# Optimization experiments

Measured on AMD Instinct MI355X. Metric: run time of the kernel, lower is better.

## Reference

```python
import jax, jax.numpy as jnp
import numpy as np

B_COEF = 1.0  # b in __init__
F_POW = 1     # f in __init__
H_POW = 2     # h in __init__
N_NODES = 16384
DIM = 16


def setup_inputs() -> dict:
    key = jax.random.key(0)
    kA, kx = jax.random.split(key)
    # Adjacency with nonnegative entries (dense, as in the torch dense branch)
    A = jax.random.uniform(kA, (N_NODES, N_NODES), dtype=jnp.float32)
    x = jax.random.uniform(kx, (N_NODES, DIM), dtype=jnp.float32)
    return {"A": A, "x": x, "t": 0}


def reference(A, x, t):
    # dx/dt = -b * x^f + (A @ x^h) / (x^h + 1)
    # NOTE: python precedence in the original: (A @ x**h) / (x**h + 1)
    xh = x ** H_POW            # [n, dim]
    agg = A @ xh               # [n, dim] adjacency aggregation
    return -B_COEF * x ** F_POW + agg / (xh + 1.0)
```

## Files before the change

kernel.cpp:

```cpp
#include <hip/hip_runtime.h>
#include <stdint.h>


#define NN 16384
#define DIM 16
#define TPB 256
#define ROWS 32
#define NRB 512
#define KSPLIT 2
#define KRANGE 8192
#define KC 256
#define NCH 32

__global__ __launch_bounds__(256) void prep_kernel(const float* __restrict__ x,
                                                   float* __restrict__ out,
                                                   float* __restrict__ xh,
                                                   float* __restrict__ inv) {
    int i = blockIdx.x * 256 + threadIdx.x;
    float4 v = reinterpret_cast<const float4*>(x)[i];
    reinterpret_cast<float4*>(out)[i] = make_float4(-v.x, -v.y, -v.z, -v.w);
    float4 h = make_float4(v.x * v.x, v.y * v.y, v.z * v.z, v.w * v.w);
    reinterpret_cast<float4*>(xh)[i] = h;
    reinterpret_cast<float4*>(inv)[i] =
        make_float4(1.0f / (h.x + 1.0f), 1.0f / (h.y + 1.0f),
                    1.0f / (h.z + 1.0f), 1.0f / (h.w + 1.0f));
}

__device__ __forceinline__ void gload_lds16(const float* g, float* l, int aux) {
    if (aux)
        __builtin_amdgcn_global_load_lds(
            (const __attribute__((address_space(1))) void*)g,
            (__attribute__((address_space(3))) void*)l, 16, 0, 2 );
    else
        __builtin_amdgcn_global_load_lds(
            (const __attribute__((address_space(1))) void*)g,
            (__attribute__((address_space(3))) void*)l, 16, 0, 0);
}

__global__ __launch_bounds__(TPB) void agg_kernel(const float* __restrict__ A,
                                                  const float* __restrict__ xh,
                                                  const float* __restrict__ inv,
                                                  float* __restrict__ out) {
    __shared__ float tA[ROWS * KC];
    __shared__ float tX[KC * DIM];

    const int tid = threadIdx.x;
    const int l = tid & 63, w = tid >> 6, m = l & 15, q = l >> 4;
    const int rb = blockIdx.x & (NRB - 1);
    const int ks = blockIdx.x >> 9;
    const int r0 = rb * ROWS;
    const size_t k0 = (size_t)ks * KRANGE;

    const float* Ab = A + (size_t)(r0 + 8 * w) * NN + k0;
    int aoff[8];
    #pragma unroll
    for (int i = 0; i < 8; ++i) aoff[i] = 4 * (l ^ (i & 7));

    const float* Xc = xh + k0 * DIM;
    int xoff[4];
    #pragma unroll
    for (int j = 0; j < 4; ++j)
        xoff[j] = (((4 * w + j) * 16 + (l >> 2)) << 4) + 4 * ((l & 3) ^ j);

    int rA[2][4];
    #pragma unroll
    for (int j = 0; j < 2; ++j)
        #pragma unroll
        for (int b = 0; b < 4; ++b)
            rA[j][b] = (m + 16 * j) * KC + 4 * ((16 * w + 4 * q + b) ^ (m & 7));
    int rX[4];
    #pragma unroll
    for (int v = 0; v < 4; ++v)
        rX[v] = (64 * w + 16 * q) * 16 + 4 * (v ^ ((4 * w + q) & 3));

    float4 acc[2][4];
    #pragma unroll
    for (int j = 0; j < 2; ++j)
        #pragma unroll
        for (int v = 0; v < 4; ++v) acc[j][v] = make_float4(0.f, 0.f, 0.f, 0.f);

    for (int t = 0; t < NCH; ++t) {
        __syncthreads();
        {
            const float* sA = Ab + (size_t)t * KC;
            #pragma unroll
            for (int i = 0; i < 8; ++i)
                gload_lds16(sA + (size_t)i * NN + aoff[i],
                            &tA[(8 * w + i) * KC], 1);
            const float* sX = Xc + (size_t)t * (KC * DIM);
            #pragma unroll
            for (int j = 0; j < 4; ++j)
                gload_lds16(sX + xoff[j], &tX[(4 * w + j) * 256], 0);
        }
        __syncthreads();
        #pragma unroll
        for (int b = 0; b < 4; ++b) {
            float4 ar[2];
            ar[0] = *reinterpret_cast<const float4*>(&tA[rA[0][b]]);
            ar[1] = *reinterpret_cast<const float4*>(&tA[rA[1][b]]);
            #pragma unroll
            for (int e = 0; e < 4; ++e) {
                float4 xv[4];
                #pragma unroll
                for (int v = 0; v < 4; ++v)
                    xv[v] = *reinterpret_cast<const float4*>(
                        &tX[rX[v] + (4 * b + e) * 16]);
                #pragma unroll
                for (int j = 0; j < 2; ++j) {
                    const float a = (&ar[j].x)[e];
                    #pragma unroll
                    for (int v = 0; v < 4; ++v) {
                        acc[j][v].x += a * xv[v].x;
                        acc[j][v].y += a * xv[v].y;
                        acc[j][v].z += a * xv[v].z;
                        acc[j][v].w += a * xv[v].w;
                    }
                }
            }
        }
    }

    #pragma unroll
    for (int j = 0; j < 2; ++j)
        #pragma unroll
        for (int v = 0; v < 4; ++v) {
            acc[j][v].x += __shfl_xor(acc[j][v].x, 16);
            acc[j][v].y += __shfl_xor(acc[j][v].y, 16);
            acc[j][v].z += __shfl_xor(acc[j][v].z, 16);
            acc[j][v].w += __shfl_xor(acc[j][v].w, 16);
            acc[j][v].x += __shfl_xor(acc[j][v].x, 32);
            acc[j][v].y += __shfl_xor(acc[j][v].y, 32);
            acc[j][v].z += __shfl_xor(acc[j][v].z, 32);
            acc[j][v].w += __shfl_xor(acc[j][v].w, 32);
        }

    if (q == 0) {
        #pragma unroll
        for (int j = 0; j < 2; ++j) {
            const int R = r0 + m + 16 * j;
            const float4* iv4 = reinterpret_cast<const float4*>(inv + (size_t)R * DIM);
            float* orow = out + (size_t)R * DIM;
            #pragma unroll
            for (int v = 0; v < 4; ++v) {
                float4 iv = iv4[v];
                atomicAdd(&orow[4 * v + 0], acc[j][v].x * iv.x);
                atomicAdd(&orow[4 * v + 1], acc[j][v].y * iv.y);
                atomicAdd(&orow[4 * v + 2], acc[j][v].z * iv.z);
                atomicAdd(&orow[4 * v + 3], acc[j][v].w * iv.w);
            }
        }
    }
}

extern "C" void kernel_launch(void* const* d_in, const int* in_sizes, int n_in,
                              void* d_out, int out_size, void* d_ws, size_t ws_size,
                              hipStream_t stream) {
    const float* A = (const float*)d_in[0];
    const float* x = (const float*)d_in[1];
    float* out = (float*)d_out;
    float* xhp = (float*)d_ws;
    float* inv = (float*)d_ws + (size_t)NN * DIM;

    prep_kernel<<<(NN * DIM / 4) / 256, 256, 0, stream>>>(x, out, xhp, inv);
    agg_kernel<<<NRB * KSPLIT, TPB, 0, stream>>>(A, xhp, inv, out);
}
```

Measured before the change: 296.1 us.

## Remap thread tile to 4 rows x 8 k-slices and use butterfly reduction

```diff
diff --git a/kernel.cpp b/kernel.cpp
--- a/kernel.cpp
+++ b/kernel.cpp
@@ -26,8 +26,8 @@
                     1.0f / (h.z + 1.0f), 1.0f / (h.w + 1.0f));
 }
 
-__device__ __forceinline__ void gload_lds16(const float* g, float* l, int aux) {
-    if (aux)
+__device__ __forceinline__ void gload_lds16(const void* g, void* l, int nt) {
+    if (nt)
         __builtin_amdgcn_global_load_lds(
             (const __attribute__((address_space(1))) void*)g,
             (__attribute__((address_space(3))) void*)l, 16, 0, 2 );
@@ -37,15 +37,23 @@
             (__attribute__((address_space(3))) void*)l, 16, 0, 0);
 }
 
-__global__ __launch_bounds__(TPB) void agg_kernel(const float* __restrict__ A,
-                                                  const float* __restrict__ xh,
-                                                  const float* __restrict__ inv,
-                                                  float* __restrict__ out) {
+__device__ __forceinline__ float4 shfl_xor4(float4 v, int mask) {
+    return make_float4(__shfl_xor(v.x, mask), __shfl_xor(v.y, mask),
+                       __shfl_xor(v.z, mask), __shfl_xor(v.w, mask));
+}
+
+__global__ __launch_bounds__(TPB)
+__attribute__((amdgpu_waves_per_eu(1, 3)))
+void agg_kernel(const float* __restrict__ A,
+                const float* __restrict__ xh,
+                const float* __restrict__ inv,
+                float* __restrict__ out) {
     __shared__ float tA[ROWS * KC];
     __shared__ float tX[KC * DIM];
 
     const int tid = threadIdx.x;
-    const int l = tid & 63, w = tid >> 6, m = l & 15, q = l >> 4;
+    const int l = tid & 63, w = tid >> 6;
+    const int m8 = l & 7, q8 = l >> 3;
     const int rb = blockIdx.x & (NRB - 1);
     const int ks = blockIdx.x >> 9;
     const int r0 = rb * ROWS;
@@ -59,23 +67,19 @@
     const float* Xc = xh + k0 * DIM;
     int xoff[4];
     #pragma unroll
+    for (int j = 0; j < 4; ++j) xoff[j] = (4 * w + j) * 256 + 4 * l;
+
+    int rA[4][2];
+    #pragma unroll
     for (int j = 0; j < 4; ++j)
-        xoff[j] = (((4 * w + j) * 16 + (l >> 2)) << 4) + 4 * ((l & 3) ^ j);
+        #pragma unroll
+        for (int b = 0; b < 2; ++b)
+            rA[j][b] = (m8 + 8 * j) * KC + 4 * ((16 * w + 2 * q8 + b) ^ m8);
+    const int XBASE = (64 * w + 8 * q8) * 16;
 
-    int rA[2][4];
+    float4 acc[4][4];
     #pragma unroll
-    for (int j = 0; j < 2; ++j)
-        #pragma unroll
-        for (int b = 0; b < 4; ++b)
-            rA[j][b] = (m + 16 * j) * KC + 4 * ((16 * w + 4 * q + b) ^ (m & 7));
-    int rX[4];
-    #pragma unroll
-    for (int v = 0; v < 4; ++v)
-        rX[v] = (64 * w + 16 * q) * 16 + 4 * (v ^ ((4 * w + q) & 3));
-
-    float4 acc[2][4];
-    #pragma unroll
-    for (int j = 0; j < 2; ++j)
+    for (int j = 0; j < 4; ++j)
         #pragma unroll
         for (int v = 0; v < 4; ++v) acc[j][v] = make_float4(0.f, 0.f, 0.f, 0.f);
 
@@ -85,8 +89,7 @@
             const float* sA = Ab + (size_t)t * KC;
             #pragma unroll
             for (int i = 0; i < 8; ++i)
-                gload_lds16(sA + (size_t)i * NN + aoff[i],
-                            &tA[(8 * w + i) * KC], 1);
+                gload_lds16(sA + (size_t)i * NN + aoff[i], &tA[(8 * w + i) * KC], 1);
             const float* sX = Xc + (size_t)t * (KC * DIM);
             #pragma unroll
             for (int j = 0; j < 4; ++j)
@@ -94,19 +97,20 @@
         }
         __syncthreads();
         #pragma unroll
-        for (int b = 0; b < 4; ++b) {
-            float4 ar[2];
-            ar[0] = *reinterpret_cast<const float4*>(&tA[rA[0][b]]);
-            ar[1] = *reinterpret_cast<const float4*>(&tA[rA[1][b]]);
+        for (int b = 0; b < 2; ++b) {
+            float4 ar[4];
+            #pragma unroll
+            for (int j = 0; j < 4; ++j)
+                ar[j] = *reinterpret_cast<const float4*>(&tA[rA[j][b]]);
             #pragma unroll
             for (int e = 0; e < 4; ++e) {
+                const int xb = XBASE + (4 * b + e) * 16;
                 float4 xv[4];
                 #pragma unroll
                 for (int v = 0; v < 4; ++v)
-                    xv[v] = *reinterpret_cast<const float4*>(
-                        &tX[rX[v] + (4 * b + e) * 16]);
+                    xv[v] = *reinterpret_cast<const float4*>(&tX[xb + 4 * v]);
                 #pragma unroll
-                for (int j = 0; j < 2; ++j) {
+                for (int j = 0; j < 4; ++j) {
                     const float a = (&ar[j].x)[e];
                     #pragma unroll
                     for (int v = 0; v < 4; ++v) {
@@ -120,35 +124,51 @@
         }
     }
 
-    #pragma unroll
-    for (int j = 0; j < 2; ++j)
+    {
+        const int b2 = (q8 >> 2) & 1, b1 = (q8 >> 1) & 1, b0 = q8 & 1;
+        #pragma unroll
+        for (int j = 0; j < 2; ++j)
+            #pragma unroll
+            for (int v = 0; v < 4; ++v) {
+                float4 send = b2 ? acc[j][v] : acc[j + 2][v];
+                float4 keep = b2 ? acc[j + 2][v] : acc[j][v];
+                float4 r = shfl_xor4(send, 32);
+                acc[j][v] = make_float4(keep.x + r.x, keep.y + r.y,
+                                        keep.z + r.z, keep.w + r.w);
+            }
         #pragma unroll
         for (int v = 0; v < 4; ++v) {
-            acc[j][v].x += __shfl_xor(acc[j][v].x, 16);
-            acc[j][v].y += __shfl_xor(acc[j][v].y, 16);
-            acc[j][v].z += __shfl_xor(acc[j][v].z, 16);
-            acc[j][v].w += __shfl_xor(acc[j][v].w, 16);
-            acc[j][v].x += __shfl_xor(acc[j][v].x, 32);
-            acc[j][v].y += __shfl_xor(acc[j][v].y, 32);
-            acc[j][v].z += __shfl_xor(acc[j][v].z, 32);
-            acc[j][v].w += __shfl_xor(acc[j][v].w, 32);
+            float4 send = b1 ? acc[0][v] : acc[1][v];
+            float4 keep = b1 ? acc[1][v] : acc[0][v];
+            float4 r = shfl_xor4(send, 16);
+            acc[0][v] = make_float4(keep.x + r.x, keep.y + r.y,
+                                    keep.z + r.z, keep.w + r.w);
         }
+        #pragma unroll
+        for (int v = 0; v < 2; ++v) {
+            float4 send = b0 ? acc[0][v] : acc[0][v + 2];
+            float4 keep = b0 ? acc[0][v + 2] : acc[0][v];
+            float4 r = shfl_xor4(send, 8);
+            acc[0][v] = make_float4(keep.x + r.x, keep.y + r.y,
+                                    keep.z + r.z, keep.w + r.w);
+        }
+    }
 
-    if (q == 0) {
-        #pragma unroll
-        for (int j = 0; j < 2; ++j) {
-            const int R = r0 + m + 16 * j;
-            const float4* iv4 = reinterpret_cast<const float4*>(inv + (size_t)R * DIM);
-            float* orow = out + (size_t)R * DIM;
-            #pragma unroll
-            for (int v = 0; v < 4; ++v) {
-                float4 iv = iv4[v];
-                atomicAdd(&orow[4 * v + 0], acc[j][v].x * iv.x);
-                atomicAdd(&orow[4 * v + 1], acc[j][v].y * iv.y);
-                atomicAdd(&orow[4 * v + 2], acc[j][v].z * iv.z);
-                atomicAdd(&orow[4 * v + 3], acc[j][v].w * iv.w);
-            }
-        }
+    {
+        const int R = r0 + m8 + 8 * (q8 >> 1);
+        const int d0 = 8 * (q8 & 1);
+        const float* ivp = inv + (size_t)R * DIM + d0;
+        float* op = out + (size_t)R * DIM + d0;
+        float4 iv0 = *reinterpret_cast<const float4*>(ivp);
+        float4 iv1 = *reinterpret_cast<const float4*>(ivp + 4);
+        atomicAdd(op + 0, acc[0][0].x * iv0.x);
+        atomicAdd(op + 1, acc[0][0].y * iv0.y);
+        atomicAdd(op + 2, acc[0][0].z * iv0.z);
+        atomicAdd(op + 3, acc[0][0].w * iv0.w);
+        atomicAdd(op + 4, acc[0][1].x * iv1.x);
+        atomicAdd(op + 5, acc[0][1].y * iv1.y);
+        atomicAdd(op + 6, acc[0][1].z * iv1.z);
+        atomicAdd(op + 7, acc[0][1].w * iv1.w);
     }
 }
 
```

Result: faster. 240.8 us, median of 2 (-18.7%).
